# Kernel tuning notes

Hardware: AMD Instinct MI355X
Metric: run time of the kernel (lower is better)

Reference implementation:

```python
import jax, jax.numpy as jnp
import numpy as np

NUM_HEADS = 12
D_MODEL = 768
D_K = D_MODEL // NUM_HEADS
B, S = 2, 4096


def setup_inputs() -> dict:
    key = jax.random.key(0)
    ks = jax.random.split(key, 11)
    s = 1.0 / np.sqrt(D_MODEL)
    inp = {
        "query": jax.random.normal(ks[0], (B, S, D_MODEL), dtype=jnp.float32),
        "key": jax.random.normal(ks[1], (B, S, D_MODEL), dtype=jnp.float32),
        "value": jax.random.normal(ks[2], (B, S, D_MODEL), dtype=jnp.float32),
        "wq": jax.random.uniform(ks[3], (D_MODEL, D_MODEL), jnp.float32, -s, s),
        "bq": jax.random.uniform(ks[4], (D_MODEL,), jnp.float32, -s, s),
        "wk": jax.random.uniform(ks[5], (D_MODEL, D_MODEL), jnp.float32, -s, s),
        "bk": jax.random.uniform(ks[6], (D_MODEL,), jnp.float32, -s, s),
        "wv": jax.random.uniform(ks[7], (D_MODEL, D_MODEL), jnp.float32, -s, s),
        "bv": jax.random.uniform(ks[8], (D_MODEL,), jnp.float32, -s, s),
        "wo": jax.random.uniform(ks[9], (D_MODEL, D_MODEL), jnp.float32, -s, s),
        "bo": jax.random.uniform(ks[10], (D_MODEL,), jnp.float32, -s, s),
    }
    return inp


def _split_heads(x):
    # [B, S, D] -> [B, H, S, d_k]
    b, s, _ = x.shape
    return x.reshape(b, s, NUM_HEADS, D_K).transpose(0, 2, 1, 3)


def reference(query, key, value, wq, bq, wk, bk, wv, bv, wo, bo):
    q = _split_heads(query @ wq.T + bq)
    k = _split_heads(key @ wk.T + bk)
    v = _split_heads(value @ wv.T + bv)
    scale = 1.0 / jnp.sqrt(jnp.asarray(D_K, q.dtype))
    scores = jnp.einsum("bhqd,bhkd->bhqk", q, k) * scale
    p = jax.nn.softmax(scores, axis=-1)
    x = jnp.einsum("bhqk,bhkd->bhqd", p, v)  # [B,H,S,d_k]
    x = x.transpose(0, 2, 1, 3).reshape(query.shape[0], -1, D_MODEL)
    return x @ wo.T + bo
```

## Files before the change

kernel.cpp:

```cpp
#include <hip/hip_runtime.h>


typedef __attribute__((ext_vector_type(8))) short short8;
typedef __attribute__((ext_vector_type(8))) unsigned short ushort8;
typedef __attribute__((ext_vector_type(4))) unsigned short bf16x4;
typedef __attribute__((ext_vector_type(4))) float f32x4;

#define SCL 0.18033688011112042f

__device__ __forceinline__ unsigned short f2bf(float f) {
    unsigned int u = __builtin_bit_cast(unsigned int, f);
    u += 0x7fffu + ((u >> 16) & 1u);
    return (unsigned short)(u >> 16);
}
__device__ __forceinline__ float bf2f(unsigned short s) {
    unsigned int u = ((unsigned int)s) << 16;
    return __builtin_bit_cast(float, u);
}

__device__ __forceinline__ void gld16(const void* g, void* l) {
    __builtin_amdgcn_global_load_lds(
        (const __attribute__((address_space(1))) unsigned int*)g,
        (__attribute__((address_space(3))) unsigned int*)l, 16, 0, 0);
}

__device__ __forceinline__ ushort8 ld8(const unsigned short* p) {
    return *(const ushort8*)p;
}
__device__ __forceinline__ ushort8 ld8(const float* p) {
    f32x4 a = *(const f32x4*)p;
    f32x4 b = *(const f32x4*)(p + 4);
    ushort8 r;
    r[0] = f2bf(a[0]); r[1] = f2bf(a[1]); r[2] = f2bf(a[2]); r[3] = f2bf(a[3]);
    r[4] = f2bf(b[0]); r[5] = f2bf(b[1]); r[6] = f2bf(b[2]); r[7] = f2bf(b[3]);
    return r;
}
__device__ __forceinline__ void st1(unsigned short* p, float v) { *p = f2bf(v); }
__device__ __forceinline__ void st1(float* p, float v)          { *p = v; }

__global__ __launch_bounds__(256) void cvt_bf16(
    const float* __restrict__ s0, unsigned short* __restrict__ d0,
    const float* __restrict__ s1, unsigned short* __restrict__ d1,
    const float* __restrict__ s2, unsigned short* __restrict__ d2,
    const float* __restrict__ s3, unsigned short* __restrict__ d3, int n)
{
    const float* s; unsigned short* d;
    if (blockIdx.y == 0)      { s = s0; d = d0; }
    else if (blockIdx.y == 1) { s = s1; d = d1; }
    else if (blockIdx.y == 2) { s = s2; d = d2; }
    else                      { s = s3; d = d3; }
    int i = (blockIdx.x * 256 + threadIdx.x) * 8;
    if (i + 8 <= n) {
        f32x4 a = *(const f32x4*)&s[i];
        f32x4 b = *(const f32x4*)&s[i + 4];
        ushort8 r;
        r[0] = f2bf(a[0]); r[1] = f2bf(a[1]); r[2] = f2bf(a[2]); r[3] = f2bf(a[3]);
        r[4] = f2bf(b[0]); r[5] = f2bf(b[1]); r[6] = f2bf(b[2]); r[7] = f2bf(b[3]);
        *(ushort8*)&d[i] = r;
    }
}

template<typename TX, typename TW, typename TY>
__global__ __launch_bounds__(256, 2) void gemm_bt(
    const TX* __restrict__ X0, const TW* __restrict__ W0,
    const float* __restrict__ B0, TY* __restrict__ Y0,
    const TX* __restrict__ X1, const TW* __restrict__ W1,
    const float* __restrict__ B1, TY* __restrict__ Y1,
    const TX* __restrict__ X2, const TW* __restrict__ W2,
    const float* __restrict__ B2, TY* __restrict__ Y2,
    int M, int N, int K, int transZ2)
{
    __shared__ __align__(16) unsigned short lds_a[128 * 32];
    __shared__ __align__(16) unsigned short lds_b[128 * 32];

    const TX *X; const TW *W; const float *Bi; TY *Y;
    if (blockIdx.z == 0)      { X = X0; W = W0; Bi = B0; Y = Y0; }
    else if (blockIdx.z == 1) { X = X1; W = W1; Bi = B1; Y = Y1; }
    else                      { X = X2; W = W2; Bi = B2; Y = Y2; }

    const int tid = threadIdx.x;
    const int wave = tid >> 6, lane = tid & 63;
    const int lane15 = lane & 15, quad = lane >> 4;
    const int m0 = blockIdx.x * 128, n0 = blockIdx.y * 128;
    const int wm = (wave & 1) * 64, wn = (wave >> 1) * 64;

    f32x4 acc[4][4] = {};

    for (int k0 = 0; k0 < K; k0 += 32) {
        __syncthreads();
#pragma unroll
        for (int i = 0; i < 2; i++) {
            int c  = tid + 256 * i;
            int r  = c >> 2;
            int c8 = (c & 3) * 8;
            if constexpr (sizeof(TX) == 2 && sizeof(TW) == 2) {
                gld16(&X[(size_t)(m0 + r) * K + k0 + c8], &lds_a[c * 8]);
                gld16(&W[(size_t)(n0 + r) * K + k0 + c8], &lds_b[c * 8]);
            } else {
                *(ushort8*)&lds_a[r * 32 + c8] = ld8(&X[(size_t)(m0 + r) * K + k0 + c8]);
                *(ushort8*)&lds_b[r * 32 + c8] = ld8(&W[(size_t)(n0 + r) * K + k0 + c8]);
            }
        }
        __syncthreads();

        short8 af[4], bfr[4];
#pragma unroll
        for (int mt = 0; mt < 4; mt++)
            af[mt] = *(const short8*)&lds_a[(wm + mt * 16 + lane15) * 32 + quad * 8];
#pragma unroll
        for (int nt = 0; nt < 4; nt++)
            bfr[nt] = *(const short8*)&lds_b[(wn + nt * 16 + lane15) * 32 + quad * 8];
#pragma unroll
        for (int mt = 0; mt < 4; mt++)
#pragma unroll
            for (int nt = 0; nt < 4; nt++)
                acc[mt][nt] = __builtin_amdgcn_mfma_f32_16x16x32_bf16(
                    af[mt], bfr[nt], acc[mt][nt], 0, 0, 0);
    }

    const bool doT = (transZ2 != 0) && (blockIdx.z == 2);
#pragma unroll
    for (int nt = 0; nt < 4; nt++) {
        int gn = n0 + wn + nt * 16 + lane15;
        float bv = Bi[gn];
        if constexpr (sizeof(TY) == 2) {
            if (doT) {
#pragma unroll
                for (int mt = 0; mt < 4; mt++) {
                    int gm = m0 + wm + mt * 16 + quad * 4;
                    bf16x4 pk;
#pragma unroll
                    for (int r = 0; r < 4; r++) pk[r] = f2bf(acc[mt][nt][r] + bv);
                    *(bf16x4*)&Y[(size_t)gn * M + gm] = pk;
                }
                continue;
            }
        }
#pragma unroll
        for (int mt = 0; mt < 4; mt++) {
            int gm = m0 + wm + mt * 16 + quad * 4;
            size_t base = (size_t)gm * N + gn;
#pragma unroll
            for (int r = 0; r < 4; r++)
                st1(&Y[base + (size_t)r * N], acc[mt][nt][r] + bv);
        }
    }
}

__global__ __launch_bounds__(256, 2) void attn(
    const unsigned short* __restrict__ Qb, const unsigned short* __restrict__ Kb,
    const unsigned short* __restrict__ Vt, unsigned short* __restrict__ Xo)
{
    const int S = 4096, D = 768, Mtot = 8192;
    __shared__ __align__(16) unsigned short lds_qp[128 * 72];
    __shared__ __align__(16) unsigned short lds_k[64 * 72];
    __shared__ __align__(16) unsigned short lds_vt[64 * 72];

    const int tid = threadIdx.x;
    const int wave = tid >> 6, lane = tid & 63;
    const int lane15 = lane & 15, quad = lane >> 4;
    const int q0 = blockIdx.x * 128;
    const int b = blockIdx.y / 12, h = blockIdx.y % 12;
    const size_t base_bh = (size_t)b * S * D + (size_t)h * 64;
    const size_t vbase   = (size_t)(h * 64) * Mtot + (size_t)b * S;

#pragma unroll
    for (int i = 0; i < 4; i++) {
        int c  = tid + 256 * i;
        int r  = c >> 3;
        int c8 = (c & 7) * 8;
        *(ushort8*)&lds_qp[r * 72 + c8] =
            *(const ushort8*)&Qb[base_bh + (size_t)(q0 + r) * D + c8];
    }
    __syncthreads();

    short8 qf[2][2];
#pragma unroll
    for (int mt = 0; mt < 2; mt++)
#pragma unroll
        for (int ks = 0; ks < 2; ks++)
            qf[mt][ks] = *(const short8*)&lds_qp[(wave * 32 + mt * 16 + lane15) * 72
                                                 + ks * 32 + quad * 8];

    f32x4 o[2][4] = {};
    float lrun[2][4] = {};

    for (int kt = 0; kt < 64; kt++) {
        const int k0 = kt * 64;
        __syncthreads();
#pragma unroll
        for (int i = 0; i < 2; i++) {
            int c  = tid + 256 * i;
            int r  = c >> 3;
            int c8 = (c & 7) * 8;
            *(ushort8*)&lds_k[r * 72 + c8] =
                *(const ushort8*)&Kb[base_bh + (size_t)(k0 + r) * D + c8];
            *(ushort8*)&lds_vt[r * 72 + c8] =
                *(const ushort8*)&Vt[vbase + (size_t)r * Mtot + k0 + c8];
        }
        __syncthreads();

        short8 kf[4][2];
#pragma unroll
        for (int nt = 0; nt < 4; nt++)
#pragma unroll
            for (int ks = 0; ks < 2; ks++)
                kf[nt][ks] = *(const short8*)&lds_k[(nt * 16 + lane15) * 72
                                                    + ks * 32 + quad * 8];
        f32x4 s[2][4];
#pragma unroll
        for (int mt = 0; mt < 2; mt++)
#pragma unroll
            for (int nt = 0; nt < 4; nt++) {
                f32x4 a = {0.f, 0.f, 0.f, 0.f};
                a = __builtin_amdgcn_mfma_f32_16x16x32_bf16(qf[mt][0], kf[nt][0], a, 0, 0, 0);
                a = __builtin_amdgcn_mfma_f32_16x16x32_bf16(qf[mt][1], kf[nt][1], a, 0, 0, 0);
                s[mt][nt] = a;
            }

#pragma unroll
        for (int mt = 0; mt < 2; mt++)
#pragma unroll
            for (int nt = 0; nt < 4; nt++)
#pragma unroll
                for (int r = 0; r < 4; r++) {
                    float p = __builtin_amdgcn_exp2f(s[mt][nt][r] * SCL);
                    unsigned short pb = f2bf(p);
                    lrun[mt][r] += bf2f(pb);
                    lds_qp[(wave * 32 + mt * 16 + quad * 4 + r) * 72 + nt * 16 + lane15] = pb;
                }
        __syncthreads();

        short8 pf[2][2], vf[4][2];
#pragma unroll
        for (int mt = 0; mt < 2; mt++)
#pragma unroll
            for (int ks = 0; ks < 2; ks++)
                pf[mt][ks] = *(const short8*)&lds_qp[(wave * 32 + mt * 16 + lane15) * 72
                                                     + ks * 32 + quad * 8];
#pragma unroll
        for (int d = 0; d < 4; d++)
#pragma unroll
            for (int ks = 0; ks < 2; ks++)
                vf[d][ks] = *(const short8*)&lds_vt[(d * 16 + lane15) * 72
                                                    + ks * 32 + quad * 8];
#pragma unroll
        for (int mt = 0; mt < 2; mt++)
#pragma unroll
            for (int d = 0; d < 4; d++) {
                o[mt][d] = __builtin_amdgcn_mfma_f32_16x16x32_bf16(pf[mt][0], vf[d][0], o[mt][d], 0, 0, 0);
                o[mt][d] = __builtin_amdgcn_mfma_f32_16x16x32_bf16(pf[mt][1], vf[d][1], o[mt][d], 0, 0, 0);
            }
    }

#pragma unroll
    for (int mt = 0; mt < 2; mt++)
#pragma unroll
        for (int r = 0; r < 4; r++) {
            float l = lrun[mt][r];
            l += __shfl_xor(l, 1);
            l += __shfl_xor(l, 2);
            l += __shfl_xor(l, 4);
            l += __shfl_xor(l, 8);
            float inv = 1.0f / l;
            int gq = q0 + wave * 32 + mt * 16 + quad * 4 + r;
            size_t rowoff = base_bh + (size_t)gq * D;
#pragma unroll
            for (int d = 0; d < 4; d++)
                Xo[rowoff + d * 16 + lane15] = f2bf(o[mt][d][r] * inv);
        }
}

extern "C" void kernel_launch(void* const* d_in, const int* in_sizes, int n_in,
                              void* d_out, int out_size, void* d_ws, size_t ws_size,
                              hipStream_t stream) {
    const float* q  = (const float*)d_in[0];
    const float* k  = (const float*)d_in[1];
    const float* v  = (const float*)d_in[2];
    const float* wq = (const float*)d_in[3];
    const float* bq = (const float*)d_in[4];
    const float* wk = (const float*)d_in[5];
    const float* bk = (const float*)d_in[6];
    const float* wv = (const float*)d_in[7];
    const float* bv = (const float*)d_in[8];
    const float* wo = (const float*)d_in[9];
    const float* bo = (const float*)d_in[10];
    float* out = (float*)d_out;

    const int M = 8192, N = 768, K = 768;
    const size_t BIG = (size_t)M * N;
    const size_t WSZ = (size_t)N * K;

    unsigned short* ws = (unsigned short*)d_ws;
    unsigned short* qb  = ws;
    unsigned short* kb  = qb + BIG;
    unsigned short* vt  = kb + BIG;
    unsigned short* xq  = vt + BIG;
    unsigned short* xk  = xq + BIG;
    unsigned short* xv  = xk + BIG;
    unsigned short* wqb = xv + BIG;
    unsigned short* wkb = wqb + WSZ;
    unsigned short* wvb = wkb + WSZ;
    unsigned short* wob = wvb + WSZ;
    unsigned short* xb  = xq;

    const size_t need = (6 * BIG + 4 * WSZ) * sizeof(unsigned short);

    if (ws_size >= need) {
        cvt_bf16<<<dim3((unsigned)(BIG / 2048), 3), 256, 0, stream>>>(
            q, xq, k, xk, v, xv, v, xv, (int)BIG);
        cvt_bf16<<<dim3((unsigned)(WSZ / 2048), 4), 256, 0, stream>>>(
            wq, wqb, wk, wkb, wv, wvb, wo, wob, (int)WSZ);

        dim3 g1(M / 128, N / 128, 3);
        gemm_bt<unsigned short, unsigned short, unsigned short>
            <<<g1, 256, 0, stream>>>(xq, wqb, bq, qb,
                                     xk, wkb, bk, kb,
                                     xv, wvb, bv, vt, M, N, K, 1);

        attn<<<dim3(4096 / 128, 2 * 12), 256, 0, stream>>>(qb, kb, vt, xb);

        dim3 g2(M / 128, N / 128, 1);
        gemm_bt<unsigned short, unsigned short, float>
            <<<g2, 256, 0, stream>>>(xb, wob, bo, out,
                                     xb, wob, bo, out,
                                     xb, wob, bo, out, M, N, K, 0);
    } else {
        unsigned short* fqb = ws;
        unsigned short* fkb = fqb + BIG;
        unsigned short* fvt = fkb + BIG;
        unsigned short* fxb = fvt + BIG;

        dim3 g1(M / 128, N / 128, 3);
        gemm_bt<float, float, unsigned short>
            <<<g1, 256, 0, stream>>>(q, wq, bq, fqb,
                                     k, wk, bk, fkb,
                                     v, wv, bv, fvt, M, N, K, 1);

        attn<<<dim3(4096 / 128, 2 * 12), 256, 0, stream>>>(fqb, fkb, fvt, fxb);

        dim3 g2(M / 128, N / 128, 1);
        gemm_bt<unsigned short, float, float>
            <<<g2, 256, 0, stream>>>(fxb, wo, bo, out,
                                     fxb, wo, bo, out,
                                     fxb, wo, bo, out, M, N, K, 0);
    }
}
```

Measured before the change: 372.2 us.

## Prefetch K/V into registers, MFMA row sums, truncate P, widen GEMM K-tile

The attention kernel now prefetches the next K/V tile into registers while the current tile is computed, computes softmax row sums with an MFMA against a ones vector instead of scalar adds plus shuffles, truncates P to bf16 instead of rounding, and drops the __syncthreads between the P writes to LDS and the P reads. The projection GEMM doubles its K-step to 64 with doubled LDS tiles and asks for 3 blocks per CU. Together these aim to cut global-load latency, barrier count and VALU work, at the cost of more registers and LDS and slightly different rounding. The removed barrier relies on each wave reading back only its own P rows, which holds here but is a fragile assumption.

```diff
diff --git a/kernel.cpp b/kernel.cpp
--- a/kernel.cpp
+++ b/kernel.cpp
@@ -12,10 +12,6 @@
     unsigned int u = __builtin_bit_cast(unsigned int, f);
     u += 0x7fffu + ((u >> 16) & 1u);
     return (unsigned short)(u >> 16);
-}
-__device__ __forceinline__ float bf2f(unsigned short s) {
-    unsigned int u = ((unsigned int)s) << 16;
-    return __builtin_bit_cast(float, u);
 }
 
 __device__ __forceinline__ void gld16(const void* g, void* l) {
@@ -61,7 +57,7 @@
 }
 
 template<typename TX, typename TW, typename TY>
-__global__ __launch_bounds__(256, 2) void gemm_bt(
+__global__ __launch_bounds__(256, 3) void gemm_bt(
     const TX* __restrict__ X0, const TW* __restrict__ W0,
     const float* __restrict__ B0, TY* __restrict__ Y0,
     const TX* __restrict__ X1, const TW* __restrict__ W1,
@@ -70,8 +66,8 @@
     const float* __restrict__ B2, TY* __restrict__ Y2,
     int M, int N, int K, int transZ2)
 {
-    __shared__ __align__(16) unsigned short lds_a[128 * 32];
-    __shared__ __align__(16) unsigned short lds_b[128 * 32];
+    __shared__ __align__(16) unsigned short lds_a[128 * 64];
+    __shared__ __align__(16) unsigned short lds_b[128 * 64];
 
     const TX *X; const TW *W; const float *Bi; TY *Y;
     if (blockIdx.z == 0)      { X = X0; W = W0; Bi = B0; Y = Y0; }
@@ -86,36 +82,45 @@
 
     f32x4 acc[4][4] = {};
 
-    for (int k0 = 0; k0 < K; k0 += 32) {
+    for (int k0 = 0; k0 < K; k0 += 64) {
         __syncthreads();
 #pragma unroll
-        for (int i = 0; i < 2; i++) {
+        for (int i = 0; i < 4; i++) {
             int c  = tid + 256 * i;
-            int r  = c >> 2;
-            int c8 = (c & 3) * 8;
+            int r  = c >> 3;
+            int c8 = (c & 7) * 8;
             if constexpr (sizeof(TX) == 2 && sizeof(TW) == 2) {
                 gld16(&X[(size_t)(m0 + r) * K + k0 + c8], &lds_a[c * 8]);
                 gld16(&W[(size_t)(n0 + r) * K + k0 + c8], &lds_b[c * 8]);
             } else {
-                *(ushort8*)&lds_a[r * 32 + c8] = ld8(&X[(size_t)(m0 + r) * K + k0 + c8]);
-                *(ushort8*)&lds_b[r * 32 + c8] = ld8(&W[(size_t)(n0 + r) * K + k0 + c8]);
+                *(ushort8*)&lds_a[r * 64 + c8] = ld8(&X[(size_t)(m0 + r) * K + k0 + c8]);
+                *(ushort8*)&lds_b[r * 64 + c8] = ld8(&W[(size_t)(n0 + r) * K + k0 + c8]);
             }
         }
         __syncthreads();
 
-        short8 af[4], bfr[4];
+        short8 af[4][2], bfr[4][2];
 #pragma unroll
         for (int mt = 0; mt < 4; mt++)
-            af[mt] = *(const short8*)&lds_a[(wm + mt * 16 + lane15) * 32 + quad * 8];
+#pragma unroll
+            for (int ks = 0; ks < 2; ks++)
+                af[mt][ks] = *(const short8*)&lds_a[(wm + mt * 16 + lane15) * 64
+                                                    + ks * 32 + quad * 8];
 #pragma unroll
         for (int nt = 0; nt < 4; nt++)
-            bfr[nt] = *(const short8*)&lds_b[(wn + nt * 16 + lane15) * 32 + quad * 8];
+#pragma unroll
+            for (int ks = 0; ks < 2; ks++)
+                bfr[nt][ks] = *(const short8*)&lds_b[(wn + nt * 16 + lane15) * 64
+                                                     + ks * 32 + quad * 8];
 #pragma unroll
         for (int mt = 0; mt < 4; mt++)
 #pragma unroll
-            for (int nt = 0; nt < 4; nt++)
+            for (int nt = 0; nt < 4; nt++) {
                 acc[mt][nt] = __builtin_amdgcn_mfma_f32_16x16x32_bf16(
-                    af[mt], bfr[nt], acc[mt][nt], 0, 0, 0);
+                    af[mt][0], bfr[nt][0], acc[mt][nt], 0, 0, 0);
+                acc[mt][nt] = __builtin_amdgcn_mfma_f32_16x16x32_bf16(
+                    af[mt][1], bfr[nt][1], acc[mt][nt], 0, 0, 0);
+            }
     }
 
     const bool doT = (transZ2 != 0) && (blockIdx.z == 2);
@@ -182,23 +187,40 @@
             qf[mt][ks] = *(const short8*)&lds_qp[(wave * 32 + mt * 16 + lane15) * 72
                                                  + ks * 32 + quad * 8];
 
+    short8 ones;
+#pragma unroll
+    for (int j = 0; j < 8; j++) ones[j] = (short)0x3F80;
+
     f32x4 o[2][4] = {};
-    float lrun[2][4] = {};
+    f32x4 lacc[2] = {};
+
+    ushort8 kreg[2], vreg[2];
+#pragma unroll
+    for (int i = 0; i < 2; i++) {
+        int c = tid + 256 * i, r = c >> 3, c8 = (c & 7) * 8;
+        kreg[i] = *(const ushort8*)&Kb[base_bh + (size_t)r * D + c8];
+        vreg[i] = *(const ushort8*)&Vt[vbase + (size_t)r * Mtot + c8];
+    }
 
     for (int kt = 0; kt < 64; kt++) {
-        const int k0 = kt * 64;
         __syncthreads();
 #pragma unroll
         for (int i = 0; i < 2; i++) {
-            int c  = tid + 256 * i;
-            int r  = c >> 3;
-            int c8 = (c & 7) * 8;
-            *(ushort8*)&lds_k[r * 72 + c8] =
-                *(const ushort8*)&Kb[base_bh + (size_t)(k0 + r) * D + c8];
-            *(ushort8*)&lds_vt[r * 72 + c8] =
-                *(const ushort8*)&Vt[vbase + (size_t)r * Mtot + k0 + c8];
+            int c = tid + 256 * i, r = c >> 3, c8 = (c & 7) * 8;
+            *(ushort8*)&lds_k[r * 72 + c8]  = kreg[i];
+            *(ushort8*)&lds_vt[r * 72 + c8] = vreg[i];
         }
         __syncthreads();
+
+        if (kt < 63) {
+            const int kn = (kt + 1) * 64;
+#pragma unroll
+            for (int i = 0; i < 2; i++) {
+                int c = tid + 256 * i, r = c >> 3, c8 = (c & 7) * 8;
+                kreg[i] = *(const ushort8*)&Kb[base_bh + (size_t)(kn + r) * D + c8];
+                vreg[i] = *(const ushort8*)&Vt[vbase + (size_t)r * Mtot + kn + c8];
+            }
+        }
 
         short8 kf[4][2];
 #pragma unroll
@@ -225,11 +247,10 @@
 #pragma unroll
                 for (int r = 0; r < 4; r++) {
                     float p = __builtin_amdgcn_exp2f(s[mt][nt][r] * SCL);
-                    unsigned short pb = f2bf(p);
-                    lrun[mt][r] += bf2f(pb);
-                    lds_qp[(wave * 32 + mt * 16 + quad * 4 + r) * 72 + nt * 16 + lane15] = pb;
+                    unsigned int u = __builtin_bit_cast(unsigned int, p);
+                    lds_qp[(wave * 32 + mt * 16 + quad * 4 + r) * 72 + nt * 16 + lane15]
+                        = (unsigned short)(u >> 16);
                 }
-        __syncthreads();
 
         short8 pf[2][2], vf[4][2];
 #pragma unroll
@@ -244,6 +265,12 @@
             for (int ks = 0; ks < 2; ks++)
                 vf[d][ks] = *(const short8*)&lds_vt[(d * 16 + lane15) * 72
                                                     + ks * 32 + quad * 8];
+
+#pragma unroll
+        for (int mt = 0; mt < 2; mt++) {
+            lacc[mt] = __builtin_amdgcn_mfma_f32_16x16x32_bf16(pf[mt][0], ones, lacc[mt], 0, 0, 0);
+            lacc[mt] = __builtin_amdgcn_mfma_f32_16x16x32_bf16(pf[mt][1], ones, lacc[mt], 0, 0, 0);
+        }
 #pragma unroll
         for (int mt = 0; mt < 2; mt++)
 #pragma unroll
@@ -257,12 +284,7 @@
     for (int mt = 0; mt < 2; mt++)
 #pragma unroll
         for (int r = 0; r < 4; r++) {
-            float l = lrun[mt][r];
-            l += __shfl_xor(l, 1);
-            l += __shfl_xor(l, 2);
-            l += __shfl_xor(l, 4);
-            l += __shfl_xor(l, 8);
-            float inv = 1.0f / l;
+            float inv = 1.0f / lacc[mt][r];
             int gq = q0 + wave * 32 + mt * 16 + quad * 4 + r;
             size_t rowoff = base_bh + (size_t)gq * D;
 #pragma unroll
```

Result: faster. 340.2 us (-8.6%).
